# Kernel tuning notes

Measured on AMD Instinct MI355X. Metric: run time of the kernel, lower is better.

## Reference

```python
import jax, jax.numpy as jnp
import numpy as np

H = 2048      # num_hidden
B = 2048      # batch_size
T = 64        # seq_length
C = 10        # num_classes


def setup_inputs() -> dict:
    key = jax.random.key(0)
    k = jax.random.split(key, 4)
    bound = float(np.sqrt(1.0 / H))  # uniform(-bound, bound) init as in the torch module
    return {
        "x": jax.random.normal(k[0], (B, T), dtype=jnp.float32),
        "W_hx": jax.random.uniform(k[1], (H, 1), jnp.float32, -bound, bound),
        "W_hh": jax.random.uniform(k[2], (H, H), jnp.float32, -bound, bound),
        "W_hy": jax.random.uniform(k[3], (H, C), jnp.float32, -bound, bound),
        "b_h": jnp.zeros((H, 1), jnp.float32),
        "b_p": jnp.zeros((C, 1), jnp.float32),
    }


def reference(x, W_hx, W_hh, W_hy, b_h, b_p):
    # x: [B, T]; hidden state kept as [H, B] to match the torch layout.
    xT = x.T  # [T, B] so scan iterates over time

    def step(h, xt):
        # W_hx @ x_t  : [H,1] @ [1,B] -> [H,B]; W_hh @ h : [H,B]
        h = jnp.tanh(W_hx @ xt[None, :] + W_hh @ h + b_h)
        return h, None

    h0 = jnp.zeros((W_hh.shape[0], x.shape[0]), x.dtype)
    hT, _ = jax.lax.scan(step, h0, xT)
    out = W_hy.T @ hT + b_p  # [C, B]
    return out.T             # [B, C]
```

## Files before the change

### kernel.cpp

```cpp
#include <hip/hip_runtime.h>
#include <cstdint>
#include <cstddef>
#include <cmath>

#define H  2048
#define BB 2048
#define TT 64
#define NC 10

typedef __bf16 bf16;
typedef bf16  bf16x8 __attribute__((ext_vector_type(8)));
typedef float f32x4  __attribute__((ext_vector_type(4)));

__device__ __forceinline__ void load_lds16(const void* g, void* l) {
    __builtin_amdgcn_global_load_lds(
        (__attribute__((address_space(1))) void*)(void*)g,
        (__attribute__((address_space(3))) void*)l,
        16, 0, 0);
}

__global__ void w_shuffle_kernel(const float* __restrict__ Whh,
                                 bf16* __restrict__ Wshuf) {
    int tid = blockIdx.x * blockDim.x + threadIdx.x;
    int sub = tid >> 6;
    int l   = tid & 63;
    int n16 = sub >> 6;
    int k32 = sub & 63;
    int n = n16 * 16 + (l & 15);
    int k = k32 * 32 + (l >> 4) * 8;
    const float* src = Whh + (size_t)n * H + k;
    bf16x8 o;
#pragma unroll
    for (int j = 0; j < 8; ++j) o[j] = (bf16)src[j];
    *(bf16x8*)(Wshuf + (size_t)tid * 8) = o;
}

__global__ void rnn_init(const float* __restrict__ x,
                         const float* __restrict__ Whx,
                         const float* __restrict__ bh,
                         bf16* __restrict__ S) {
    int b  = blockIdx.x;
    int i0 = threadIdx.x * 8;
    float xv = x[(size_t)b * TT];
    bf16x8 o;
#pragma unroll
    for (int j = 0; j < 8; ++j)
        o[j] = (bf16)tanhf(Whx[i0 + j] * xv + bh[i0 + j]);
    size_t sub  = (size_t)(b >> 4) * 64 + (i0 >> 5);
    size_t slot = (size_t)(b & 15) | (size_t)(((i0 >> 3) & 3) << 4);
    *(bf16x8*)(S + (sub * 64 + slot) * 8) = o;
}

#define PH_WAIT(NSTR) asm volatile("s_waitcnt vmcnt(" NSTR ")" ::: "memory")
#define SBAR0()       __builtin_amdgcn_sched_barrier(0)

__launch_bounds__(512, 2)
__global__ void rnn_step(const float* __restrict__ x,
                         const float* __restrict__ Whx,
                         const float* __restrict__ bh,
                         const bf16*  __restrict__ Wshuf,
                         const bf16*  __restrict__ Sr,
                         bf16* __restrict__ Sw,
                         int t) {
    __shared__ __align__(16) char Ls[4][32768];

    const int tid  = threadIdx.x;
    const int w    = tid >> 6;
    const int lane = tid & 63;
    const int lrow = lane & 15;
    const int quad = lane >> 4;

    const int xcd = blockIdx.x & 7;
    const int loc = blockIdx.x >> 3;
    const int bm0 = (loc >> 1) * 128;
    const int bn0 = xcd * 256 + (loc & 1) * 128;

    const int kh   = w >> 2;
    const int s    = w & 3;
    const int qm   = s & 1;
    const int qn   = s >> 1;
    const int cn0  = bn0 + qn * 64;
    const int kh16 = kh * 16;

    const char* srcA = (const char*)Sr +
        ((size_t)((bm0 >> 4) + w) * 64) * 1024 + (size_t)lane * 16;
    const char* srcB = (const char*)Wshuf +
        ((size_t)((bn0 >> 4) + w) * 64) * 1024 + (size_t)lane * 16;

    f32x4 acc[4][4];
#pragma unroll
    for (int i = 0; i < 4; ++i)
#pragma unroll
        for (int j = 0; j < 4; ++j) acc[i][j] = (f32x4){0.f, 0.f, 0.f, 0.f};

#define ISSUE(RI, pp)                                                        \
    {                                                                        \
        load_lds16(srcA + (size_t)(pp) * 1024,        &Ls[RI][w * 1024]);    \
        load_lds16(srcB + (size_t)(pp) * 1024,        &Ls[RI][(8 + w) * 1024]); \
        load_lds16(srcA + (size_t)(32 + (pp)) * 1024, &Ls[RI][(16 + w) * 1024]); \
        load_lds16(srcB + (size_t)(32 + (pp)) * 1024, &Ls[RI][(24 + w) * 1024]); \
    }

#define COMPUTE(RI)                                                          \
    {                                                                        \
        bf16x8 Af[4], Bf[4];                                                 \
        _Pragma("unroll")                                                    \
        for (int fm = 0; fm < 4; ++fm)                                       \
            Af[fm] = *(const bf16x8*)&Ls[RI]                                 \
                [(kh16 + qm * 4 + fm) * 1024 + lane * 16];                   \
        _Pragma("unroll")                                                    \
        for (int fn = 0; fn < 4; ++fn)                                       \
            Bf[fn] = *(const bf16x8*)&Ls[RI]                                 \
                [(kh16 + 8 + qn * 4 + fn) * 1024 + lane * 16];               \
        __builtin_amdgcn_s_setprio(1);                                       \
        _Pragma("unroll")                                                    \
        for (int fm = 0; fm < 4; ++fm)                                       \
            _Pragma("unroll")                                                \
            for (int fn = 0; fn < 4; ++fn)                                   \
                acc[fm][fn] = __builtin_amdgcn_mfma_f32_16x16x32_bf16(       \
                    Af[fm], Bf[fn], acc[fm][fn], 0, 0, 0);                   \
        __builtin_amdgcn_s_setprio(0);                                       \
    }

#define PHASE(RI, RN, p, WNSTR, DOISS)                                       \
    {                                                                        \
        PH_WAIT(WNSTR);                                                      \
        SBAR0();                                                             \
        __builtin_amdgcn_s_barrier();                                        \
        SBAR0();                                                             \
        if (DOISS) ISSUE(RN, (p) + 3);                                       \
        SBAR0();                                                             \
        COMPUTE(RI);                                                         \
    }

    ISSUE(0, 0); SBAR0();
    ISSUE(1, 1); SBAR0();
    ISSUE(2, 2); SBAR0();

#pragma unroll 1
    for (int q = 0; q < 7; ++q) {
        int p = 4 * q;
        PHASE(0, 3, p + 0, "8", true);
        PHASE(1, 0, p + 1, "8", true);
        PHASE(2, 1, p + 2, "8", true);
        PHASE(3, 2, p + 3, "8", true);
    }
    PHASE(0, 3, 28, "8", true);
    PHASE(1, 0, 29, "8", false);
    PHASE(2, 1, 30, "4", false);
    PHASE(3, 2, 31, "0", false);

#undef PHASE
#undef COMPUTE
#undef ISSUE

    char* red = &Ls[0][0];
    const int pairbase = s * 16384;
    if (kh == 0) {
#pragma unroll
        for (int fml = 0; fml < 2; ++fml)
#pragma unroll
            for (int fn = 0; fn < 4; ++fn)
                *(f32x4*)&red[pairbase + (fml * 4 + fn) * 1024 + lane * 16] =
                    acc[2 + fml][fn];
    } else {
#pragma unroll
        for (int fml = 0; fml < 2; ++fml)
#pragma unroll
            for (int fn = 0; fn < 4; ++fn)
                *(f32x4*)&red[pairbase + 8192 + (fml * 4 + fn) * 1024 +
                              lane * 16] = acc[fml][fn];
    }
    __syncthreads();
    f32x4 own[2][4];
    if (kh == 0) {
#pragma unroll
        for (int fml = 0; fml < 2; ++fml)
#pragma unroll
            for (int fn = 0; fn < 4; ++fn)
                own[fml][fn] = acc[fml][fn] + *(const f32x4*)&red[pairbase +
                    8192 + (fml * 4 + fn) * 1024 + lane * 16];
    } else {
#pragma unroll
        for (int fml = 0; fml < 2; ++fml)
#pragma unroll
            for (int fn = 0; fn < 4; ++fn)
                own[fml][fn] = acc[2 + fml][fn] + *(const f32x4*)&red[pairbase +
                    (fml * 4 + fn) * 1024 + lane * 16];
    }

    bf16* Lw = (bf16*)&Ls[2][0] + (size_t)w * 2048;
#pragma unroll
    for (int fml = 0; fml < 2; ++fml) {
        int rb = bm0 + qm * 64 + (kh * 2 + fml) * 16 + quad * 4;
        float xv[4];
#pragma unroll
        for (int r = 0; r < 4; ++r) xv[r] = x[(size_t)(rb + r) * TT + t];
#pragma unroll
        for (int fn = 0; fn < 4; ++fn) {
            int col = cn0 + fn * 16 + lrow;
            float wx = Whx[col], bb = bh[col];
            int cbyte = (fn * 16 + lrow) * 2;
#pragma unroll
            for (int r = 0; r < 4; ++r) {
                int row_l = fml * 16 + quad * 4 + r;
                float z = own[fml][fn][r] + wx * xv[r] + bb;
                *(bf16*)((char*)Lw + row_l * 128 +
                         (cbyte ^ ((row_l & 7) << 4))) = (bf16)tanhf(z);
            }
        }
    }
#pragma unroll
    for (int fml = 0; fml < 2; ++fml) {
#pragma unroll
        for (int kc = 0; kc < 2; ++kc) {
            int row_l = fml * 16 + lrow;
            int cb    = (kc * 64 + quad * 16) ^ ((row_l & 7) << 4);
            bf16x8 v = *(const bf16x8*)((const char*)Lw + row_l * 128 + cb);
            size_t sub = (size_t)((bm0 >> 4) + qm * 4 + kh * 2 + fml) * 64 +
                         (cn0 >> 5) + kc;
            *(bf16x8*)(Sw + (sub * 64 + lane) * 8) = v;
        }
    }
}

__global__ void out_proj(const bf16* __restrict__ S,
                         const float* __restrict__ Why,
                         const float* __restrict__ bp,
                         float* __restrict__ out) {
    int b = blockIdx.x, tid = threadIdx.x;
    int h0 = tid * 8;
    size_t sub  = (size_t)(b >> 4) * 64 + (h0 >> 5);
    size_t slot = (size_t)(b & 15) | (size_t)(((h0 >> 3) & 3) << 4);
    bf16x8 v = *(const bf16x8*)(S + (sub * 64 + slot) * 8);
    float p[NC];
#pragma unroll
    for (int c = 0; c < NC; ++c) p[c] = 0.f;
#pragma unroll
    for (int j = 0; j < 8; ++j) {
        float s = (float)v[j];
        const float* wr = Why + (size_t)(h0 + j) * NC;
#pragma unroll
        for (int c = 0; c < NC; ++c) p[c] += s * wr[c];
    }
    __shared__ float red[256 * NC];
#pragma unroll
    for (int c = 0; c < NC; ++c) red[tid * NC + c] = p[c];
    __syncthreads();
    for (int s = 128; s > 0; s >>= 1) {
        if (tid < s)
#pragma unroll
            for (int c = 0; c < NC; ++c) red[tid * NC + c] += red[(tid + s) * NC + c];
        __syncthreads();
    }
    if (tid < NC) out[(size_t)b * NC + tid] = red[tid] + bp[tid];
}

extern "C" void kernel_launch(void* const* d_in, const int* in_sizes, int n_in,
                              void* d_out, int out_size, void* d_ws, size_t ws_size,
                              hipStream_t stream) {
    const float* x   = (const float*)d_in[0];
    const float* Whx = (const float*)d_in[1];
    const float* Whh = (const float*)d_in[2];
    const float* Why = (const float*)d_in[3];
    const float* bh  = (const float*)d_in[4];
    const float* bp  = (const float*)d_in[5];
    float* out = (float*)d_out;

    bf16* Wshuf = (bf16*)d_ws;
    bf16* S0 = (bf16*)((char*)d_ws + (size_t)8 * 1024 * 1024);
    bf16* S1 = (bf16*)((char*)d_ws + (size_t)16 * 1024 * 1024);

    hipLaunchKernelGGL(w_shuffle_kernel, dim3((H * H / 8) / 256), dim3(256),
                       0, stream, Whh, Wshuf);

    hipLaunchKernelGGL(rnn_init, dim3(BB), dim3(256), 0, stream, x, Whx, bh, S1);

    for (int t = 1; t < TT; ++t) {
        const bf16* Srd = (t & 1) ? S1 : S0;
        bf16*       Swr = (t & 1) ? S0 : S1;
        hipLaunchKernelGGL(rnn_step, dim3(256), dim3(512), 0, stream,
                           x, Whx, bh, Wshuf, Srd, Swr, t);
    }

    hipLaunchKernelGGL(out_proj, dim3(BB), dim3(256), 0, stream, S0, Why, bp, out);
}
```

Measured before the change: 1.526 ms.

## Double-buffer LDS fragment reads in registers to overlap with MFMAs

Splits each pipeline phase into an LDS-to-register read for the next stage and MFMAs on fragments already held in registers, using ping-pong register sets. The aim is to hide ds_read latency behind the matrix instructions instead of stalling before each MFMA block. The vmcnt waits and the prologue are adjusted to match. The change costs extra VGPRs for the second fragment set, which may lower occupancy.

Measured after the change: 1.469 ms (median of 2 runs). 3.7% less time.

```diff
diff --git a/kernel.cpp b/kernel.cpp
--- a/kernel.cpp
+++ b/kernel.cpp
@@ -93,6 +93,8 @@
 #pragma unroll
         for (int j = 0; j < 4; ++j) acc[i][j] = (f32x4){0.f, 0.f, 0.f, 0.f};
 
+    bf16x8 Ae[4], Be[4], Ao[4], Bo[4];
+
 #define ISSUE(RI, pp)                                                        \
     {                                                                        \
         load_lds16(srcA + (size_t)(pp) * 1024,        &Ls[RI][w * 1024]);    \
@@ -101,57 +103,66 @@
         load_lds16(srcB + (size_t)(32 + (pp)) * 1024, &Ls[RI][(24 + w) * 1024]); \
     }
 
-#define COMPUTE(RI)                                                          \
-    {                                                                        \
-        bf16x8 Af[4], Bf[4];                                                 \
+#define DSREAD(Ax, Bx, RI)                                                   \
+    {                                                                        \
         _Pragma("unroll")                                                    \
         for (int fm = 0; fm < 4; ++fm)                                       \
-            Af[fm] = *(const bf16x8*)&Ls[RI]                                 \
+            Ax[fm] = *(const bf16x8*)&Ls[RI]                                 \
                 [(kh16 + qm * 4 + fm) * 1024 + lane * 16];                   \
         _Pragma("unroll")                                                    \
         for (int fn = 0; fn < 4; ++fn)                                       \
-            Bf[fn] = *(const bf16x8*)&Ls[RI]                                 \
+            Bx[fn] = *(const bf16x8*)&Ls[RI]                                 \
                 [(kh16 + 8 + qn * 4 + fn) * 1024 + lane * 16];               \
+    }
+
+#define MFMAS(Ax, Bx)                                                        \
+    {                                                                        \
         __builtin_amdgcn_s_setprio(1);                                       \
         _Pragma("unroll")                                                    \
         for (int fm = 0; fm < 4; ++fm)                                       \
             _Pragma("unroll")                                                \
             for (int fn = 0; fn < 4; ++fn)                                   \
                 acc[fm][fn] = __builtin_amdgcn_mfma_f32_16x16x32_bf16(       \
-                    Af[fm], Bf[fn], acc[fm][fn], 0, 0, 0);                   \
+                    Ax[fm], Bx[fn], acc[fm][fn], 0, 0, 0);                   \
         __builtin_amdgcn_s_setprio(0);                                       \
     }
 
-#define PHASE(RI, RN, p, WNSTR, DOISS)                                       \
-    {                                                                        \
-        PH_WAIT(WNSTR);                                                      \
+#define PHASE(RNext, RIss, p, W, DOISS, DOREAD, AN, BN, AC, BC)              \
+    {                                                                        \
+        PH_WAIT(W);                                                          \
         SBAR0();                                                             \
         __builtin_amdgcn_s_barrier();                                        \
         SBAR0();                                                             \
-        if (DOISS) ISSUE(RN, (p) + 3);                                       \
-        SBAR0();                                                             \
-        COMPUTE(RI);                                                         \
+        if (DOISS) ISSUE(RIss, (p) + 3);                                     \
+        if (DOREAD) DSREAD(AN, BN, RNext);                                   \
+        MFMAS(AC, BC);                                                       \
     }
 
     ISSUE(0, 0); SBAR0();
     ISSUE(1, 1); SBAR0();
     ISSUE(2, 2); SBAR0();
+    PH_WAIT("8");
+    SBAR0();
+    __builtin_amdgcn_s_barrier();
+    SBAR0();
+    DSREAD(Ae, Be, 0);
 
 #pragma unroll 1
     for (int q = 0; q < 7; ++q) {
         int p = 4 * q;
-        PHASE(0, 3, p + 0, "8", true);
-        PHASE(1, 0, p + 1, "8", true);
-        PHASE(2, 1, p + 2, "8", true);
-        PHASE(3, 2, p + 3, "8", true);
-    }
-    PHASE(0, 3, 28, "8", true);
-    PHASE(1, 0, 29, "8", false);
-    PHASE(2, 1, 30, "4", false);
-    PHASE(3, 2, 31, "0", false);
+        PHASE(1, 3, p + 0, "4", 1, 1, Ao, Bo, Ae, Be);
+        PHASE(2, 0, p + 1, "4", 1, 1, Ae, Be, Ao, Bo);
+        PHASE(3, 1, p + 2, "4", 1, 1, Ao, Bo, Ae, Be);
+        PHASE(0, 2, p + 3, "4", 1, 1, Ae, Be, Ao, Bo);
+    }
+    PHASE(1, 3, 28, "4", 1, 1, Ao, Bo, Ae, Be);
+    PHASE(2, 0, 29, "4", 0, 1, Ae, Be, Ao, Bo);
+    PHASE(3, 1, 30, "0", 0, 1, Ao, Bo, Ae, Be);
+    PHASE(0, 2, 31, "0", 0, 0, Ae, Be, Ao, Bo);
 
 #undef PHASE
-#undef COMPUTE
+#undef MFMAS
+#undef DSREAD
 #undef ISSUE
 
     char* red = &Ls[0][0];
```

## Ping-pong warp groups alternating MFMA and LDS reads with larger per-warp tiles

Applied to the files above, without the earlier changes.

Restructures the per-step GEMM so that the eight waves form two groups that take turns: while one group issues MFMAs on the current LDS buffer, the other preloads its fragments for the next buffer. Each wave now owns a 128x64 tile (8x4 MFMA fragments) over a quarter of the K range, which changes the load mapping and requires a multi-stage cross-wave reduction through LDS before the tanh epilogue. The goal is to overlap LDS reads with matrix-core work and to reuse each fragment across more MFMAs. In exchange the doubled accumulators raise register pressure, and the reduction adds extra LDS traffic and barriers.

New measurement: 1.615 ms. 5.9% more time.

```diff
diff --git a/kernel.cpp b/kernel.cpp
--- a/kernel.cpp
+++ b/kernel.cpp
@@ -75,46 +75,56 @@
     const int bm0 = (loc >> 1) * 128;
     const int bn0 = xcd * 256 + (loc & 1) * 128;
 
-    const int kh   = w >> 2;
-    const int s    = w & 3;
-    const int qm   = s & 1;
-    const int qn   = s >> 1;
-    const int cn0  = bn0 + qn * 64;
-    const int kh16 = kh * 16;
+    const int nq  = w & 1;
+    const int kq  = w >> 1;
+    const int khi = kq >> 1;
+    const int dlt = kq & 1;
+    const int cn0 = bn0 + nq * 64;
 
     const char* srcA = (const char*)Sr +
         ((size_t)((bm0 >> 4) + w) * 64) * 1024 + (size_t)lane * 16;
     const char* srcB = (const char*)Wshuf +
         ((size_t)((bn0 >> 4) + w) * 64) * 1024 + (size_t)lane * 16;
 
-    f32x4 acc[4][4];
-#pragma unroll
-    for (int i = 0; i < 4; ++i)
+    f32x4 acc[8][4];
+#pragma unroll
+    for (int i = 0; i < 8; ++i)
 #pragma unroll
         for (int j = 0; j < 4; ++j) acc[i][j] = (f32x4){0.f, 0.f, 0.f, 0.f};
+
+    bf16x8 Af[8], Bf[4];
 
 #define ISSUE(RI, pp)                                                        \
     {                                                                        \
-        load_lds16(srcA + (size_t)(pp) * 1024,        &Ls[RI][w * 1024]);    \
-        load_lds16(srcB + (size_t)(pp) * 1024,        &Ls[RI][(8 + w) * 1024]); \
-        load_lds16(srcA + (size_t)(32 + (pp)) * 1024, &Ls[RI][(16 + w) * 1024]); \
-        load_lds16(srcB + (size_t)(32 + (pp)) * 1024, &Ls[RI][(24 + w) * 1024]); \
-    }
-
-#define COMPUTE(RI)                                                          \
+        const int qa_ = 2 * ((pp) & 1);                                      \
+        const int cc_ = (pp) >> 1;                                           \
+        load_lds16(srcA + (size_t)(qa_ * 16 + cc_) * 1024,                   \
+                   &Ls[RI][w * 1024]);                                       \
+        load_lds16(srcA + (size_t)((qa_ + 1) * 16 + cc_) * 1024,             \
+                   &Ls[RI][(8 + w) * 1024]);                                 \
+        load_lds16(srcB + (size_t)(qa_ * 16 + cc_) * 1024,                   \
+                   &Ls[RI][(16 + w) * 1024]);                                \
+        load_lds16(srcB + (size_t)((qa_ + 1) * 16 + cc_) * 1024,             \
+                   &Ls[RI][(24 + w) * 1024]);                                \
+    }
+
+#define DSREAD(RI)                                                           \
     {                                                                        \
-        bf16x8 Af[4], Bf[4];                                                 \
         _Pragma("unroll")                                                    \
-        for (int fm = 0; fm < 4; ++fm)                                       \
+        for (int fm = 0; fm < 8; ++fm)                                       \
             Af[fm] = *(const bf16x8*)&Ls[RI]                                 \
-                [(kh16 + qm * 4 + fm) * 1024 + lane * 16];                   \
+                [(dlt * 8 + fm) * 1024 + lane * 16];                         \
         _Pragma("unroll")                                                    \
         for (int fn = 0; fn < 4; ++fn)                                       \
             Bf[fn] = *(const bf16x8*)&Ls[RI]                                 \
-                [(kh16 + 8 + qn * 4 + fn) * 1024 + lane * 16];               \
+                [(16 + dlt * 8 + nq * 4 + fn) * 1024 + lane * 16];           \
+    }
+
+#define MFMAS()                                                              \
+    {                                                                        \
         __builtin_amdgcn_s_setprio(1);                                       \
         _Pragma("unroll")                                                    \
-        for (int fm = 0; fm < 4; ++fm)                                       \
+        for (int fm = 0; fm < 8; ++fm)                                       \
             _Pragma("unroll")                                                \
             for (int fn = 0; fn < 4; ++fn)                                   \
                 acc[fm][fn] = __builtin_amdgcn_mfma_f32_16x16x32_bf16(       \
@@ -122,77 +132,123 @@
         __builtin_amdgcn_s_setprio(0);                                       \
     }
 
-#define PHASE(RI, RN, p, WNSTR, DOISS)                                       \
+#define PHASE(RNext, RIss, p, W, DOISS, PARITY, DOREAD)                      \
     {                                                                        \
-        PH_WAIT(WNSTR);                                                      \
-        SBAR0();                                                             \
-        __builtin_amdgcn_s_barrier();                                        \
-        SBAR0();                                                             \
-        if (DOISS) ISSUE(RN, (p) + 3);                                       \
-        SBAR0();                                                             \
-        COMPUTE(RI);                                                         \
+        PH_WAIT(W); SBAR0();                                                 \
+        __builtin_amdgcn_s_barrier(); SBAR0();                               \
+        if (DOISS) ISSUE(RIss, (p) + 3);                                     \
+        if (khi == (PARITY)) { MFMAS(); }                                    \
+        else if (DOREAD) { DSREAD(RNext); }                                  \
     }
 
     ISSUE(0, 0); SBAR0();
     ISSUE(1, 1); SBAR0();
     ISSUE(2, 2); SBAR0();
+    PH_WAIT("8"); SBAR0();
+    __builtin_amdgcn_s_barrier(); SBAR0();
+    if (khi == 0) DSREAD(0);
 
 #pragma unroll 1
     for (int q = 0; q < 7; ++q) {
         int p = 4 * q;
-        PHASE(0, 3, p + 0, "8", true);
-        PHASE(1, 0, p + 1, "8", true);
-        PHASE(2, 1, p + 2, "8", true);
-        PHASE(3, 2, p + 3, "8", true);
-    }
-    PHASE(0, 3, 28, "8", true);
-    PHASE(1, 0, 29, "8", false);
-    PHASE(2, 1, 30, "4", false);
-    PHASE(3, 2, 31, "0", false);
+        PHASE(1, 3, p + 0, "4", 1, 0, 1);
+        PHASE(2, 0, p + 1, "4", 1, 1, 1);
+        PHASE(3, 1, p + 2, "4", 1, 0, 1);
+        PHASE(0, 2, p + 3, "4", 1, 1, 1);
+    }
+    PHASE(1, 3, 28, "4", 1, 0, 1);
+    PHASE(2, 0, 29, "4", 0, 1, 1);
+    PHASE(3, 1, 30, "0", 0, 0, 1);
+    PHASE(0, 2, 31, "0", 0, 1, 0);
 
 #undef PHASE
-#undef COMPUTE
+#undef MFMAS
+#undef DSREAD
 #undef ISSUE
 
     char* red = &Ls[0][0];
-    const int pairbase = s * 16384;
-    if (kh == 0) {
+    if (kq == 1 || kq == 3) {
+        char* r0 = red + (size_t)(nq * 2 + khi) * 32768;
+#pragma unroll
+        for (int fm = 0; fm < 8; ++fm)
+#pragma unroll
+            for (int fn = 0; fn < 4; ++fn)
+                *(f32x4*)&r0[((fm * 4 + fn) * 64 + lane) * 16] = acc[fm][fn];
+    }
+    __syncthreads();
+    if (kq == 0 || kq == 2) {
+        const char* r0 = red + (size_t)(nq * 2 + khi) * 32768;
+#pragma unroll
+        for (int fm = 0; fm < 8; ++fm)
+#pragma unroll
+            for (int fn = 0; fn < 4; ++fn)
+                acc[fm][fn] += *(const f32x4*)&r0[((fm * 4 + fn) * 64 + lane) * 16];
+    }
+    __syncthreads();
+    if (kq == 0) {
+        char* r2 = red + (size_t)(nq * 2 + 0) * 24576;
 #pragma unroll
         for (int fml = 0; fml < 2; ++fml)
 #pragma unroll
-            for (int fn = 0; fn < 4; ++fn)
-                *(f32x4*)&red[pairbase + (fml * 4 + fn) * 1024 + lane * 16] =
-                    acc[2 + fml][fn];
-    } else {
+            for (int fn = 0; fn < 4; ++fn) {
+                *(f32x4*)&r2[0 * 8192 + ((fml * 4 + fn) * 64 + lane) * 16] = acc[2 + fml][fn];
+                *(f32x4*)&r2[1 * 8192 + ((fml * 4 + fn) * 64 + lane) * 16] = acc[4 + fml][fn];
+                *(f32x4*)&r2[2 * 8192 + ((fml * 4 + fn) * 64 + lane) * 16] = acc[6 + fml][fn];
+            }
+    } else if (kq == 2) {
+        char* r2 = red + (size_t)(nq * 2 + 1) * 24576;
 #pragma unroll
         for (int fml = 0; fml < 2; ++fml)
 #pragma unroll
-            for (int fn = 0; fn < 4; ++fn)
-                *(f32x4*)&red[pairbase + 8192 + (fml * 4 + fn) * 1024 +
-                              lane * 16] = acc[fml][fn];
+            for (int fn = 0; fn < 4; ++fn) {
+                *(f32x4*)&r2[0 * 8192 + ((fml * 4 + fn) * 64 + lane) * 16] = acc[0 + fml][fn];
+                *(f32x4*)&r2[1 * 8192 + ((fml * 4 + fn) * 64 + lane) * 16] = acc[2 + fml][fn];
+                *(f32x4*)&r2[2 * 8192 + ((fml * 4 + fn) * 64 + lane) * 16] = acc[6 + fml][fn];
+            }
     }
     __syncthreads();
     f32x4 own[2][4];
-    if (kh == 0) {
-#pragma unroll
-        for (int fml = 0; fml < 2; ++fml)
-#pragma unroll
-            for (int fn = 0; fn < 4; ++fn)
-                own[fml][fn] = acc[fml][fn] + *(const f32x4*)&red[pairbase +
-                    8192 + (fml * 4 + fn) * 1024 + lane * 16];
-    } else {
-#pragma unroll
-        for (int fml = 0; fml < 2; ++fml)
-#pragma unroll
-            for (int fn = 0; fn < 4; ++fn)
-                own[fml][fn] = acc[2 + fml][fn] + *(const f32x4*)&red[pairbase +
-                    (fml * 4 + fn) * 1024 + lane * 16];
-    }
-
-    bf16* Lw = (bf16*)&Ls[2][0] + (size_t)w * 2048;
+    {
+        const char* rA = red + (size_t)(nq * 2 + 0) * 24576;
+        const char* rB = red + (size_t)(nq * 2 + 1) * 24576;
+        if (kq == 0) {
+#pragma unroll
+            for (int fml = 0; fml < 2; ++fml)
+#pragma unroll
+                for (int fn = 0; fn < 4; ++fn)
+                    own[fml][fn] = acc[fml][fn] +
+                        *(const f32x4*)&rB[0 * 8192 + ((fml * 4 + fn) * 64 + lane) * 16];
+        } else if (kq == 1) {
+#pragma unroll
+            for (int fml = 0; fml < 2; ++fml)
+#pragma unroll
+                for (int fn = 0; fn < 4; ++fn)
+                    own[fml][fn] =
+                        *(const f32x4*)&rA[0 * 8192 + ((fml * 4 + fn) * 64 + lane) * 16] +
+                        *(const f32x4*)&rB[1 * 8192 + ((fml * 4 + fn) * 64 + lane) * 16];
+        } else if (kq == 2) {
+#pragma unroll
+            for (int fml = 0; fml < 2; ++fml)
+#pragma unroll
+                for (int fn = 0; fn < 4; ++fn)
+                    own[fml][fn] = acc[4 + fml][fn] +
+                        *(const f32x4*)&rA[1 * 8192 + ((fml * 4 + fn) * 64 + lane) * 16];
+        } else {
+#pragma unroll
+            for (int fml = 0; fml < 2; ++fml)
+#pragma unroll
+                for (int fn = 0; fn < 4; ++fn)
+                    own[fml][fn] =
+                        *(const f32x4*)&rA[2 * 8192 + ((fml * 4 + fn) * 64 + lane) * 16] +
+                        *(const f32x4*)&rB[2 * 8192 + ((fml * 4 + fn) * 64 + lane) * 16];
+        }
+    }
+    __syncthreads();
+
+    bf16* Lw = (bf16*)&Ls[0][0] + (size_t)w * 2048;
 #pragma unroll
     for (int fml = 0; fml < 2; ++fml) {
-        int rb = bm0 + qm * 64 + (kh * 2 + fml) * 16 + quad * 4;
+        int rb = bm0 + (kq * 2 + fml) * 16 + quad * 4;
         float xv[4];
 #pragma unroll
         for (int r = 0; r < 4; ++r) xv[r] = x[(size_t)(rb + r) * TT + t];
@@ -217,7 +273,7 @@
             int row_l = fml * 16 + lrow;
             int cb    = (kc * 64 + quad * 16) ^ ((row_l & 7) << 4);
             bf16x8 v = *(const bf16x8*)((const char*)Lw + row_l * 128 + cb);
-            size_t sub = (size_t)((bm0 >> 4) + qm * 4 + kh * 2 + fml) * 64 +
+            size_t sub = (size_t)((bm0 >> 4) + kq * 2 + fml) * 64 +
                          (cn0 >> 5) + kc;
             *(bf16x8*)(Sw + (sub * 64 + lane) * 8) = v;
         }
```
